# Kernel optimization log

Measured on AMD Instinct MI355X. Metric: run time of the kernel, lower is better.

Reference implementation:

```python
import jax, jax.numpy as jnp
import numpy as np
from jax import lax
from jax.scipy.special import logsumexp

S, B, H, T = 512, 128, 512, 48  # seq_len, batch, hidden_dim, tagset_size


def setup_inputs() -> dict:
    key = jax.random.key(0)
    k1, k2, k3, k4 = jax.random.split(key, 4)
    word_features = jax.random.normal(k1, (S, B, H), dtype=jnp.float32)
    W = jax.random.normal(k2, (T, H), dtype=jnp.float32) * 0.02  # linear_layer weight
    b = jnp.zeros((T,), dtype=jnp.float32)                        # linear_layer bias
    transitions = jax.random.normal(k3, (T, T), dtype=jnp.float32) * 0.01
    tags = jax.random.randint(k4, (S, B), 0, T, dtype=jnp.int32)
    return {"word_features": word_features, "W": W, "b": b,
            "transitions": transitions, "tags": tags}


def reference(word_features, W, b, transitions, tags):
    # CRFScore: emissions[s,b,t] = Linear(word_features); crf_scores[s,b,i,j] = emissions[s,b,j] + transitions[i,j]
    emissions = jnp.einsum('sbh,th->sbt', word_features, W) + b  # [S,B,T]

    # Forward algorithm (partition function) via serial logsumexp scan over time.
    def step(alpha, emit_t):
        # alpha: [B,T] log-scores ending at tag i; expand over to-tag j
        new_alpha = logsumexp(alpha[:, :, None] + transitions[None, :, :], axis=1) + emit_t
        return new_alpha, None

    alpha0 = emissions[0]                       # [B,T]
    alphaT, _ = lax.scan(step, alpha0, emissions[1:])
    log_Z = logsumexp(alphaT, axis=1)           # [B]

    # Gold path score: sum of gold emissions + gold transitions
    em_gold = jnp.take_along_axis(emissions, tags[:, :, None], axis=2)[..., 0].sum(axis=0)  # [B]
    tr_gold = transitions[tags[:-1], tags[1:]].sum(axis=0)                                   # [B]
    gold_score = em_gold + tr_gold

    # Negative log-likelihood averaged over batch
    nll = jnp.mean(log_Z - gold_score)
    return nll
```

## Files before the change

kernel.cpp:

```cpp
#include <hip/hip_runtime.h>
#include <math.h>

#define S_DIM 512
#define B_DIM 128
#define H_DIM 512
#define T_DIM 48

typedef short bf16x8 __attribute__((ext_vector_type(8)));
typedef short s16x4  __attribute__((ext_vector_type(4)));
typedef float f32x4  __attribute__((ext_vector_type(4)));

__device__ __forceinline__ short rne_bf(float f) {
  unsigned u = __float_as_uint(f);
  u += 0x7fffu + ((u >> 16) & 1u);
  return (short)(u >> 16);
}
__device__ __forceinline__ short trunc_bf(float f) {
  return (short)(__float_as_uint(f) >> 16);
}
__device__ __forceinline__ bf16x8 cvt8(const float* __restrict__ p) {
  float4 v0 = *(const float4*)p, v1 = *(const float4*)(p + 4);
  bf16x8 r;
  r[0] = rne_bf(v0.x); r[1] = rne_bf(v0.y); r[2] = rne_bf(v0.z); r[3] = rne_bf(v0.w);
  r[4] = rne_bf(v1.x); r[5] = rne_bf(v1.y); r[6] = rne_bf(v1.z); r[7] = rne_bf(v1.w);
  return r;
}

struct Frags6 { bf16x8 b[2][3]; };

__device__ __forceinline__ void load_child(const short* __restrict__ p, int h, int q, Frags6& f) {
  bf16x8 z = 0;
#pragma unroll
  for (int ct = 0; ct < 3; ++ct) {
    const short* col = p + (16 * ct + q) * 48;
    f.b[0][ct] = *(const bf16x8*)(col + 8 * h);
    f.b[1][ct] = (h < 2) ? *(const bf16x8*)(col + 32 + 8 * h) : z;
  }
}

__device__ __forceinline__ void matstep(const short* Ml, bool useI, int h, int q,
                                        const Frags6& B, f32x4 C[3][3]) {
  const f32x4 Z = {0.f, 0.f, 0.f, 0.f};
#pragma unroll
  for (int rt = 0; rt < 3; ++rt) {
    const int row = 16 * rt + q;
    bf16x8 a0, a1;
    if (useI) {
      const short one = (short)0x3F80;
#pragma unroll
      for (int i = 0; i < 8; ++i) {
        a0[i] = (row == 8 * h + i) ? one : (short)0;
        a1[i] = (row == 32 + 8 * h + i) ? one : (short)0;
      }
    } else {
      const int sw = (row & 7) << 3;
      a0 = *(const bf16x8*)&Ml[row * 64 + ((8 * h) ^ sw)];
      a1 = *(const bf16x8*)&Ml[row * 64 + ((32 + 8 * h) ^ sw)];
    }
#pragma unroll
    for (int ct = 0; ct < 3; ++ct)
      C[rt][ct] = __builtin_amdgcn_mfma_f32_16x16x32_bf16(
          a1, B.b[1][ct],
          __builtin_amdgcn_mfma_f32_16x16x32_bf16(a0, B.b[0][ct], Z, 0, 0, 0), 0, 0, 0);
  }
}

__device__ __forceinline__ void writeM(short* Ml, int h, int q, const f32x4 C[3][3]) {
#pragma unroll
  for (int rt = 0; rt < 3; ++rt)
#pragma unroll
    for (int ct = 0; ct < 3; ++ct) {
      const int j = 16 * ct + q;
#pragma unroll
      for (int r = 0; r < 4; ++r) {
        const int row = 16 * rt + 4 * h + r;
        Ml[row * 64 + (j ^ ((row & 7) << 3))] = trunc_bf(C[rt][ct][r]);
      }
    }
}

__device__ __forceinline__ void storecol(short* __restrict__ node, int h, int q,
                                         const f32x4 C[3][3]) {
#pragma unroll
  for (int rt = 0; rt < 3; ++rt)
#pragma unroll
    for (int ct = 0; ct < 3; ++ct) {
      s16x4 pk;
#pragma unroll
      for (int r = 0; r < 4; ++r) pk[r] = rne_bf(C[rt][ct][r]);
      *(s16x4*)&node[(16 * ct + q) * 48 + 16 * rt + 4 * h] = pk;
    }
}

__device__ __forceinline__ int rescaleC(f32x4 C[3][3]) {
  float mx = 0.f;
#pragma unroll
  for (int rt = 0; rt < 3; ++rt)
#pragma unroll
    for (int ct = 0; ct < 3; ++ct)
#pragma unroll
      for (int r = 0; r < 4; ++r) mx = fmaxf(mx, C[rt][ct][r]);
#pragma unroll
  for (int off = 1; off < 64; off <<= 1) mx = fmaxf(mx, __shfl_xor(mx, off, 64));
  int ex;
  frexpf(mx, &ex);
  const float sc = ldexpf(1.0f, -ex);
#pragma unroll
  for (int rt = 0; rt < 3; ++rt)
#pragma unroll
    for (int ct = 0; ct < 3; ++ct)
#pragma unroll
      for (int r = 0; r < 4; ++r) C[rt][ct][r] *= sc;
  return ex;
}

__device__ __forceinline__ int store_node(short* __restrict__ node, int h, int q,
                                          f32x4 C[3][3]) {
  int ex = rescaleC(C);
  storecol(node, h, q, C);
  return ex;
}

__device__ __forceinline__ void zero_lds(short* Ml, int l) {
  s16x4 z = 0;
#pragma unroll
  for (int i = 0; i < 12; ++i) *(s16x4*)&Ml[(l + 64 * i) * 4] = z;
}

__global__ __launch_bounds__(256) void k_emissions(
    const float* __restrict__ wf, const float* __restrict__ W,
    const float* __restrict__ bias, float* __restrict__ em,
    float* __restrict__ out) {
  if (blockIdx.x == 0 && threadIdx.x == 0) out[0] = 0.0f;
  const int tid = threadIdx.x;
  const int w = tid >> 6, l = tid & 63, h = l >> 4, q = l & 15;
  const size_t r0 = (size_t)blockIdx.x * 128;

  f32x4 C[2][3];
#pragma unroll
  for (int rt = 0; rt < 2; ++rt)
#pragma unroll
    for (int ct = 0; ct < 3; ++ct) C[rt][ct] = 0.f;

  for (int ks = 0; ks < 16; ++ks) {
    const int k0 = 32 * ks + 8 * h;
    bf16x8 a[2], bb[3];
#pragma unroll
    for (int rt = 0; rt < 2; ++rt)
      a[rt] = cvt8(&wf[(r0 + 32 * w + 16 * rt + q) * H_DIM + k0]);
#pragma unroll
    for (int ct = 0; ct < 3; ++ct)
      bb[ct] = cvt8(&W[(size_t)(16 * ct + q) * H_DIM + k0]);
#pragma unroll
    for (int rt = 0; rt < 2; ++rt)
#pragma unroll
      for (int ct = 0; ct < 3; ++ct)
        C[rt][ct] = __builtin_amdgcn_mfma_f32_16x16x32_bf16(a[rt], bb[ct], C[rt][ct], 0, 0, 0);
  }
  float bv[3];
#pragma unroll
  for (int ct = 0; ct < 3; ++ct) bv[ct] = bias[16 * ct + q];
#pragma unroll
  for (int rt = 0; rt < 2; ++rt)
#pragma unroll
    for (int ct = 0; ct < 3; ++ct)
#pragma unroll
      for (int r = 0; r < 4; ++r) {
        const size_t row = r0 + 32 * w + 16 * rt + 4 * h + r;
        em[row * T_DIM + 16 * ct + q] = C[rt][ct][r] + bv[ct];
      }
}

__global__ __launch_bounds__(64) void k_tree1(
    const float* __restrict__ em, const float* __restrict__ trans,
    short* __restrict__ nodes1, int* __restrict__ exp1) {
  const int b = blockIdx.x >> 5, c = blockIdx.x & 31;
  const int l = threadIdx.x, h = l >> 4, q = l & 15;
  __shared__ short Ml[48 * 64];
  zero_lds(Ml, l);

  Frags6 B;
#pragma unroll
  for (int ct = 0; ct < 3; ++ct) {
    const int j = 16 * ct + q;
#pragma unroll
    for (int i = 0; i < 8; ++i) {
      const int k0 = 8 * h + i;
      B.b[0][ct][i] = rne_bf(__expf(trans[k0 * T_DIM + j]));
      const int k1 = 32 + 8 * h + i;
      B.b[1][ct][i] = (k1 < T_DIM) ? rne_bf(__expf(trans[k1 * T_DIM + j])) : (short)0;
    }
  }

  const int s0 = 1 + 16 * c;
  const int NT = min(16, 511 - 16 * c);
  size_t ro = (size_t)(s0 * B_DIM + b) * T_DIM;
  float eA0 = __expf(em[ro + q]), eA1 = __expf(em[ro + 16 + q]), eA2 = __expf(em[ro + 32 + q]);
  float eB0 = 0.f, eB1 = 0.f, eB2 = 0.f;

  f32x4 C[3][3];
  for (int t = 0; t < NT; ++t) {
    if (t + 1 < NT) {
      size_t rn = (size_t)((s0 + t + 1) * B_DIM + b) * T_DIM;
      eB0 = __expf(em[rn + q]); eB1 = __expf(em[rn + 16 + q]); eB2 = __expf(em[rn + 32 + q]);
    }
    matstep(Ml, t == 0, h, q, B, C);
#pragma unroll
    for (int rt = 0; rt < 3; ++rt)
#pragma unroll
      for (int r = 0; r < 4; ++r) {
        C[rt][0][r] *= eA0; C[rt][1][r] *= eA1; C[rt][2][r] *= eA2;
      }
    writeM(Ml, h, q, C);
    eA0 = eB0; eA1 = eB1; eA2 = eB2;
  }
  int ex = store_node(nodes1 + (size_t)(b * 32 + c) * 2304, h, q, C);
  if (l == 0) exp1[b * 32 + c] = ex;
}

__global__ __launch_bounds__(256) void k_final(
    const short* __restrict__ nodes1, const int* __restrict__ exp1,
    const float* __restrict__ em, const float* __restrict__ trans,
    const int* __restrict__ tags, float* __restrict__ out) {
  const int b = blockIdx.x, tid = threadIdx.x;
  const int v = tid >> 6, l = tid & 63, h = l >> 4, q = l & 15;
  __shared__ short Ml[4][48 * 64];
  __shared__ short Pc[3][2304];
  __shared__ float gred[4];
  __shared__ int wexp[4];

  float g = 0.f;
  for (int s = tid; s < S_DIM; s += 256) {
    const int tg = tags[s * B_DIM + b];
    g += em[(size_t)(s * B_DIM + b) * T_DIM + tg];
    if (s < S_DIM - 1) g += trans[tg * T_DIM + tags[(s + 1) * B_DIM + b]];
  }
#pragma unroll
  for (int off = 1; off < 64; off <<= 1) g += __shfl_xor(g, off, 64);
  if (l == 0) gred[v] = g;

  zero_lds(Ml[v], l);
  const short* base = nodes1 + (size_t)(b * 32 + 8 * v) * 2304;
  Frags6 B, Bn;
  load_child(base, h, q, B);
  f32x4 C[3][3];
  for (int t = 0; t < 8; ++t) {
    if (t < 7) load_child(base + (size_t)(t + 1) * 2304, h, q, Bn);
    matstep(Ml[v], t == 0, h, q, B, C);
    if (t < 7) { writeM(Ml[v], h, q, C); B = Bn; }
  }
  int ex = rescaleC(C);
  if (l == 0) wexp[v] = ex;
  if (v > 0) storecol(Pc[v - 1], h, q, C);
  else       writeM(Ml[0], h, q, C);
  __syncthreads();

  if (v == 0) {
    for (int t = 0; t < 3; ++t) {
      load_child(Pc[t], h, q, B);
      matstep(Ml[0], false, h, q, B, C);
      if (t < 2) writeM(Ml[0], h, q, C);
    }
    float Zp = 0.f;
#pragma unroll
    for (int rt = 0; rt < 3; ++rt)
#pragma unroll
      for (int r = 0; r < 4; ++r) {
        float rs = C[rt][0][r] + C[rt][1][r] + C[rt][2][r];
        rs += __shfl_xor(rs, 1, 64); rs += __shfl_xor(rs, 2, 64);
        rs += __shfl_xor(rs, 4, 64); rs += __shfl_xor(rs, 8, 64);
        const int row = 16 * rt + 4 * h + r;
        Zp = fmaf(__expf(em[(size_t)b * T_DIM + row]), rs, Zp);
      }
    Zp += __shfl_xor(Zp, 16, 64); Zp += __shfl_xor(Zp, 32, 64);
    int E = (l < 32) ? exp1[b * 32 + l] : 0;
#pragma unroll
    for (int off = 1; off < 32; off <<= 1) E += __shfl_xor(E, off, 64);
    E += wexp[0] + wexp[1] + wexp[2] + wexp[3];
    const float logZ = __logf(Zp) + (float)E * 0.69314718055994531f;
    const float gold = gred[0] + gred[1] + gred[2] + gred[3];
    if (l == 0) atomicAdd(out, (logZ - gold) * (1.0f / (float)B_DIM));
  }
}

extern "C" void kernel_launch(void* const* d_in, const int* in_sizes, int n_in,
                              void* d_out, int out_size, void* d_ws, size_t ws_size,
                              hipStream_t stream) {
  const float* wf    = (const float*)d_in[0];
  const float* W     = (const float*)d_in[1];
  const float* bias  = (const float*)d_in[2];
  const float* trans = (const float*)d_in[3];
  const int*   tags  = (const int*)d_in[4];
  float* out = (float*)d_out;

  char* p = (char*)d_ws;
  float* em     = (float*)p;  p += (size_t)S_DIM * B_DIM * T_DIM * 4;
  short* nodes1 = (short*)p;  p += (size_t)128 * 32 * 2304 * 2;
  int*   exp1   = (int*)p;

  k_emissions<<<512, 256, 0, stream>>>(wf, W, bias, em, out);
  k_tree1<<<128 * 32, 64, 0, stream>>>(em, trans, nodes1, exp1);
  k_final<<<128, 256, 0, stream>>>(nodes1, exp1, em, trans, tags, out);
}
```

Measured before the change: 253.8 us.

## Fuse emission GEMM into per-chunk tree kernel and feed emissions via shuffles

Merges the emissions GEMM and the first-level chunk product kernel into one launch. Each 64-thread block now computes the 16 emission rows it needs with MFMA, writes them to global memory for the final kernel, and passes them to the matrix-product loop through wave shuffles instead of reloading them. The chunk boundaries move to cover steps 16c..16c+15, with chunk 0 skipping step 0. This removes a launch and the em round trip, but the GEMM becomes a strided per-batch gather done by small blocks, and W is reloaded by every block.

```diff
diff --git a/kernel.cpp b/kernel.cpp
--- a/kernel.cpp
+++ b/kernel.cpp
@@ -127,57 +127,43 @@
   for (int i = 0; i < 12; ++i) *(s16x4*)&Ml[(l + 64 * i) * 4] = z;
 }
 
-__global__ __launch_bounds__(256) void k_emissions(
+__global__ __launch_bounds__(64) void k_fused(
     const float* __restrict__ wf, const float* __restrict__ W,
-    const float* __restrict__ bias, float* __restrict__ em,
+    const float* __restrict__ bias, const float* __restrict__ trans,
+    float* __restrict__ em, short* __restrict__ nodes1, int* __restrict__ exp1,
     float* __restrict__ out) {
-  if (blockIdx.x == 0 && threadIdx.x == 0) out[0] = 0.0f;
-  const int tid = threadIdx.x;
-  const int w = tid >> 6, l = tid & 63, h = l >> 4, q = l & 15;
-  const size_t r0 = (size_t)blockIdx.x * 128;
-
-  f32x4 C[2][3];
-#pragma unroll
-  for (int rt = 0; rt < 2; ++rt)
-#pragma unroll
-    for (int ct = 0; ct < 3; ++ct) C[rt][ct] = 0.f;
+  const int b = blockIdx.x >> 5, c = blockIdx.x & 31;
+  const int l = threadIdx.x, h = l >> 4, q = l & 15;
+  if (blockIdx.x == 0 && l == 0) out[0] = 0.0f;
+
+  const int s0 = 16 * c;
+  f32x4 E[3];
+#pragma unroll
+  for (int ct = 0; ct < 3; ++ct) E[ct] = 0.f;
 
   for (int ks = 0; ks < 16; ++ks) {
     const int k0 = 32 * ks + 8 * h;
-    bf16x8 a[2], bb[3];
-#pragma unroll
-    for (int rt = 0; rt < 2; ++rt)
-      a[rt] = cvt8(&wf[(r0 + 32 * w + 16 * rt + q) * H_DIM + k0]);
+    bf16x8 a = cvt8(&wf[((size_t)(s0 + q) * B_DIM + b) * H_DIM + k0]);
+    bf16x8 bb[3];
 #pragma unroll
     for (int ct = 0; ct < 3; ++ct)
       bb[ct] = cvt8(&W[(size_t)(16 * ct + q) * H_DIM + k0]);
 #pragma unroll
-    for (int rt = 0; rt < 2; ++rt)
-#pragma unroll
-      for (int ct = 0; ct < 3; ++ct)
-        C[rt][ct] = __builtin_amdgcn_mfma_f32_16x16x32_bf16(a[rt], bb[ct], C[rt][ct], 0, 0, 0);
-  }
-  float bv[3];
-#pragma unroll
-  for (int ct = 0; ct < 3; ++ct) bv[ct] = bias[16 * ct + q];
-#pragma unroll
-  for (int rt = 0; rt < 2; ++rt)
-#pragma unroll
-    for (int ct = 0; ct < 3; ++ct)
-#pragma unroll
-      for (int r = 0; r < 4; ++r) {
-        const size_t row = r0 + 32 * w + 16 * rt + 4 * h + r;
-        em[row * T_DIM + 16 * ct + q] = C[rt][ct][r] + bv[ct];
-      }
-}
-
-__global__ __launch_bounds__(64) void k_tree1(
-    const float* __restrict__ em, const float* __restrict__ trans,
-    short* __restrict__ nodes1, int* __restrict__ exp1) {
-  const int b = blockIdx.x >> 5, c = blockIdx.x & 31;
-  const int l = threadIdx.x, h = l >> 4, q = l & 15;
-  __shared__ short Ml[48 * 64];
-  zero_lds(Ml, l);
+    for (int ct = 0; ct < 3; ++ct)
+      E[ct] = __builtin_amdgcn_mfma_f32_16x16x32_bf16(a, bb[ct], E[ct], 0, 0, 0);
+  }
+#pragma unroll
+  for (int ct = 0; ct < 3; ++ct) {
+    const float bv = bias[16 * ct + q];
+#pragma unroll
+    for (int r = 0; r < 4; ++r) E[ct][r] += bv;
+  }
+#pragma unroll
+  for (int r = 0; r < 4; ++r) {
+    const size_t ro = ((size_t)(s0 + 4 * h + r) * B_DIM + b) * T_DIM;
+#pragma unroll
+    for (int ct = 0; ct < 3; ++ct) em[ro + 16 * ct + q] = E[ct][r];
+  }
 
   Frags6 B;
 #pragma unroll
@@ -192,27 +178,26 @@
     }
   }
 
-  const int s0 = 1 + 16 * c;
-  const int NT = min(16, 511 - 16 * c);
-  size_t ro = (size_t)(s0 * B_DIM + b) * T_DIM;
-  float eA0 = __expf(em[ro + q]), eA1 = __expf(em[ro + 16 + q]), eA2 = __expf(em[ro + 32 + q]);
-  float eB0 = 0.f, eB1 = 0.f, eB2 = 0.f;
+  __shared__ short Ml[48 * 64];
+  zero_lds(Ml, l);
+  const int tstart = (c == 0) ? 1 : 0;
 
   f32x4 C[3][3];
-  for (int t = 0; t < NT; ++t) {
-    if (t + 1 < NT) {
-      size_t rn = (size_t)((s0 + t + 1) * B_DIM + b) * T_DIM;
-      eB0 = __expf(em[rn + q]); eB1 = __expf(em[rn + 16 + q]); eB2 = __expf(em[rn + 32 + q]);
-    }
-    matstep(Ml, t == 0, h, q, B, C);
+#pragma unroll
+  for (int t = 0; t < 16; ++t) {
+    if (t < tstart) continue;
+    const int src = 16 * (t >> 2) + q;
+    const float e0 = __expf(__shfl(E[0][t & 3], src, 64));
+    const float e1 = __expf(__shfl(E[1][t & 3], src, 64));
+    const float e2 = __expf(__shfl(E[2][t & 3], src, 64));
+    matstep(Ml, t == tstart, h, q, B, C);
 #pragma unroll
     for (int rt = 0; rt < 3; ++rt)
 #pragma unroll
       for (int r = 0; r < 4; ++r) {
-        C[rt][0][r] *= eA0; C[rt][1][r] *= eA1; C[rt][2][r] *= eA2;
-      }
-    writeM(Ml, h, q, C);
-    eA0 = eB0; eA1 = eB1; eA2 = eB2;
+        C[rt][0][r] *= e0; C[rt][1][r] *= e1; C[rt][2][r] *= e2;
+      }
+    if (t < 15) writeM(Ml, h, q, C);
   }
   int ex = store_node(nodes1 + (size_t)(b * 32 + c) * 2304, h, q, C);
   if (l == 0) exp1[b * 32 + c] = ex;
@@ -298,7 +283,6 @@
   short* nodes1 = (short*)p;  p += (size_t)128 * 32 * 2304 * 2;
   int*   exp1   = (int*)p;
 
-  k_emissions<<<512, 256, 0, stream>>>(wf, W, bias, em, out);
-  k_tree1<<<128 * 32, 64, 0, stream>>>(em, trans, nodes1, exp1);
+  k_fused<<<128 * 32, 64, 0, stream>>>(wf, W, bias, trans, em, nodes1, exp1, out);
   k_final<<<128, 256, 0, stream>>>(nodes1, exp1, em, trans, tags, out);
 }
```

Measured after the change: 261.6 us. 1.03x slower.
